# Kernel tuning notes

Hardware: AMD Instinct MI355X
Metric: run time of the kernel (lower is better)

## Reference

```python
import jax, jax.numpy as jnp
import numpy as np

N_NODES = 100000
N_EDGES = 3200000
IN_C, HID_C, OUT_C = 5, 128, 64


def setup_inputs() -> dict:
    key = jax.random.key(0)
    k_x, k_e, k_w1, k_b1, k_w2, k_b2 = jax.random.split(key, 6)
    x = jax.random.normal(k_x, (N_NODES, IN_C), dtype=jnp.float32)
    edge_index = jax.random.randint(k_e, (2, N_EDGES), 0, N_NODES, dtype=jnp.int32)
    # GCNConv learned params (glorot weights, zero-ish bias)
    W1 = jax.random.normal(k_w1, (IN_C, HID_C), dtype=jnp.float32) * (1.0 / np.sqrt(IN_C))
    b1 = jax.random.normal(k_b1, (HID_C,), dtype=jnp.float32) * 0.01
    W2 = jax.random.normal(k_w2, (HID_C, OUT_C), dtype=jnp.float32) * (1.0 / np.sqrt(HID_C))
    b2 = jax.random.normal(k_b2, (OUT_C,), dtype=jnp.float32) * 0.01
    return {"x": x, "edge_index": edge_index, "W1": W1, "b1": b1, "W2": W2, "b2": b2}


def _gcn_conv(x, src, dst, deg_inv_sqrt, W, b):
    """One GCNConv (PyG defaults: self-loops already in src/dst, symmetric norm, bias)."""
    h = x @ W                                   # [N, C_out]
    norm = deg_inv_sqrt[src] * deg_inv_sqrt[dst]  # [E+N]
    msg = h[src] * norm[:, None]                # gather + scale
    out = jax.ops.segment_sum(msg, dst, num_segments=x.shape[0])  # scatter-add
    return out + b


def reference(x, edge_index, W1, b1, W2, b2):
    n = x.shape[0]
    loop = jnp.arange(n, dtype=edge_index.dtype)
    src = jnp.concatenate([edge_index[0], loop])  # self-loops appended
    dst = jnp.concatenate([edge_index[1], loop])
    deg = jax.ops.segment_sum(jnp.ones_like(src, dtype=x.dtype), dst, num_segments=n)
    deg_inv_sqrt = jnp.where(deg > 0, jax.lax.rsqrt(deg), 0.0)
    h = _gcn_conv(x, src, dst, deg_inv_sqrt, W1, b1)
    z = _gcn_conv(h, src, dst, deg_inv_sqrt, W2, b2)
    return z
```

## Files before the change

kernel.cpp:

```cpp
#include <hip/hip_runtime.h>

#define IN_C  5
#define HID_C 128
#define OUT_C 64

#define KB   256
#define NBP  512
#define CAP  10240
#define TILE 4096
#define BTH  512
#define EPT  (TILE / BTH)
#define GNODES 64


__global__ __launch_bounds__(BTH) void k_bin(const int* __restrict__ src,
                                             const int* __restrict__ dstp,
                                             int* __restrict__ gcursor,
                                             int* __restrict__ binned, int e) {
    __shared__ int lhist[NBP];
    __shared__ int lfill[NBP];
    __shared__ int lgofs[NBP];
    __shared__ int lbeg[NBP];
    __shared__ int lsort[TILE];
    __shared__ int gdst[TILE];
    __shared__ int wsum[8];
    __shared__ int stot;
    int tid = threadIdx.x;
    int lane = tid & 63, w = tid >> 6;
    int tbeg = blockIdx.x * TILE;
    lhist[tid] = 0; lfill[tid] = 0;
    __syncthreads();
    int pk[EPT], bk[EPT];
    #pragma unroll
    for (int q = 0; q < EPT; ++q) {
        int idx = tbeg + q * BTH + tid;
        if (idx < e) {
            int s = src[idx], d = dstp[idx];
            pk[q] = ((d & 255) << 24) | s;
            bk[q] = ((unsigned)d) >> 8;
            atomicAdd(&lhist[bk[q]], 1);
        } else bk[q] = -1;
    }
    __syncthreads();
    int h = lhist[tid];
    int v = h;
    #pragma unroll
    for (int m = 1; m < 64; m <<= 1) { int u = __shfl_up(v, m); if (lane >= m) v += u; }
    if (lane == 63) wsum[w] = v;
    __syncthreads();
    if (tid == 0) {
        int s = 0;
        #pragma unroll
        for (int k = 0; k < 8; ++k) { int tv = wsum[k]; wsum[k] = s; s += tv; }
    }
    __syncthreads();
    int excl = wsum[w] + v - h;
    lbeg[tid] = excl;
    if (h > 0)
        lgofs[tid] = tid * CAP + atomicAdd(&gcursor[tid], h) - excl;
    if (tid == BTH - 1) stot = excl + h;
    __syncthreads();
    #pragma unroll
    for (int q = 0; q < EPT; ++q) {
        if (bk[q] >= 0) {
            int slot = lbeg[bk[q]] + atomicAdd(&lfill[bk[q]], 1);
            lsort[slot] = pk[q];
            gdst[slot] = lgofs[bk[q]] + slot;
        }
    }
    __syncthreads();
    int tot = stot;
    for (int i = tid; i < tot; i += BTH)
        binned[gdst[i]] = lsort[i];
}

__global__ __launch_bounds__(BTH) void k_build(int* __restrict__ binned,
                                               const int* __restrict__ gcursor,
                                               const float* __restrict__ x,
                                               int2* __restrict__ pse,
                                               float* __restrict__ xs, int n) {
    __shared__ int cnt[KB];
    __shared__ int wt[4];
    __shared__ int wte[4];
    int tid = threadIdx.x;
    int lane = tid & 63, w = tid >> 6;
    int bkt = blockIdx.x;
    int beg = bkt * CAP;
    int tot = gcursor[bkt];
    if (tid < KB) cnt[tid] = 0;
    __syncthreads();
    int4 r[5];
    #pragma unroll
    for (int it = 0; it < 5; ++it) {
        int j0 = (tid << 2) + it * (BTH * 4);
        if (j0 < tot) {
            r[it] = *(const int4*)(binned + beg + j0);
            atomicAdd(&cnt[((unsigned)r[it].x) >> 24], 1);
            if (j0 + 1 < tot) atomicAdd(&cnt[((unsigned)r[it].y) >> 24], 1);
            if (j0 + 2 < tot) atomicAdd(&cnt[((unsigned)r[it].z) >> 24], 1);
            if (j0 + 3 < tot) atomicAdd(&cnt[((unsigned)r[it].w) >> 24], 1);
        }
    }
    __syncthreads();
    int deg = (tid < KB) ? cnt[tid] : 0;
    int v = deg;
    #pragma unroll
    for (int m = 1; m < 64; m <<= 1) { int u = __shfl_up(v, m); if (lane >= m) v += u; }
    if (tid < KB && lane == 63) wt[w] = v;
    __syncthreads();
    if (tid == 0) {
        int s = 0;
        #pragma unroll
        for (int k = 0; k < 4; ++k) { wte[k] = s; s += wt[k]; }
    }
    __syncthreads();
    if (tid < KB) {
        int rel = wte[w] + v - deg;
        int node = bkt * KB + tid;
        pse[node] = make_int2(beg + rel, beg + rel + deg);
        cnt[tid] = rel;
        float d = rsqrtf(1.0f + (float)deg);
        float4 q0 = {0, 0, 0, 0}, q1 = {0, 0, 0, 0};
        if (node < n) {
            q0.x = x[node * IN_C + 0] * d;
            q0.y = x[node * IN_C + 1] * d;
            q0.z = x[node * IN_C + 2] * d;
            q0.w = x[node * IN_C + 3] * d;
            q1.x = x[node * IN_C + 4] * d;
            q1.y = d;
        }
        ((float4*)(xs + (size_t)node * 8))[0] = q0;
        ((float4*)(xs + (size_t)node * 8))[1] = q1;
    }
    __syncthreads();
    #pragma unroll
    for (int it = 0; it < 5; ++it) {
        int j0 = (tid << 2) + it * (BTH * 4);
        if (j0 < tot) {
            {
                int slot = atomicAdd(&cnt[((unsigned)r[it].x) >> 24], 1);
                binned[beg + slot] = r[it].x & 0xFFFFFF;
            }
            if (j0 + 1 < tot) {
                int slot = atomicAdd(&cnt[((unsigned)r[it].y) >> 24], 1);
                binned[beg + slot] = r[it].y & 0xFFFFFF;
            }
            if (j0 + 2 < tot) {
                int slot = atomicAdd(&cnt[((unsigned)r[it].z) >> 24], 1);
                binned[beg + slot] = r[it].z & 0xFFFFFF;
            }
            if (j0 + 3 < tot) {
                int slot = atomicAdd(&cnt[((unsigned)r[it].w) >> 24], 1);
                binned[beg + slot] = r[it].w & 0xFFFFFF;
            }
        }
    }
}

__global__ __launch_bounds__(BTH) void k_gath0(const int* __restrict__ srclist,
                                               const int2* __restrict__ pse,
                                               const float* __restrict__ feat,
                                               float* __restrict__ outf,
                                               float* __restrict__ tout, int n) {
    int tid = threadIdx.x;
    int node = blockIdx.x * GNODES + (tid >> 3);
    int sub = tid & 7;
    if (node >= n) return;
    int2 pp = pse[node];
    int ps = pp.x, pe = pp.y;
    float a0 = 0, a1 = 0, a2 = 0, a3 = 0, a4 = 0, a5 = 0;
    int j = ps + sub;
    for (; j + 24 < pe; j += 32) {
        int s0 = srclist[j],      s1 = srclist[j + 8];
        int s2 = srclist[j + 16], s3 = srclist[j + 24];
        const float* b0 = feat + (size_t)s0 * 8;
        const float* b1 = feat + (size_t)s1 * 8;
        const float* b2 = feat + (size_t)s2 * 8;
        const float* b3 = feat + (size_t)s3 * 8;
        float4 rA0 = *(const float4*)b0; float2 rA1 = *(const float2*)(b0 + 4);
        float4 rB0 = *(const float4*)b1; float2 rB1 = *(const float2*)(b1 + 4);
        float4 rC0 = *(const float4*)b2; float2 rC1 = *(const float2*)(b2 + 4);
        float4 rD0 = *(const float4*)b3; float2 rD1 = *(const float2*)(b3 + 4);
        a0 += (rA0.x + rB0.x) + (rC0.x + rD0.x);
        a1 += (rA0.y + rB0.y) + (rC0.y + rD0.y);
        a2 += (rA0.z + rB0.z) + (rC0.z + rD0.z);
        a3 += (rA0.w + rB0.w) + (rC0.w + rD0.w);
        a4 += (rA1.x + rB1.x) + (rC1.x + rD1.x);
        a5 += (rA1.y + rB1.y) + (rC1.y + rD1.y);
    }
    for (; j < pe; j += 8) {
        int sA = srclist[j];
        const float* bA = feat + (size_t)sA * 8;
        float4 rA0 = *(const float4*)bA; float2 rA1 = *(const float2*)(bA + 4);
        a0 += rA0.x; a1 += rA0.y; a2 += rA0.z; a3 += rA0.w;
        a4 += rA1.x; a5 += rA1.y;
    }
    #pragma unroll
    for (int m = 1; m < 8; m <<= 1) {
        a0 += __shfl_xor(a0, m);
        a1 += __shfl_xor(a1, m);
        a2 += __shfl_xor(a2, m);
        a3 += __shfl_xor(a3, m);
        a4 += __shfl_xor(a4, m);
        a5 += __shfl_xor(a5, m);
    }
    if (sub == 0) {
        const float4* psr = (const float4*)(feat + (size_t)node * 8);
        float4 s0 = psr[0], s1 = psr[1];
        float d = s1.y;
        a0 += s0.x; a1 += s0.y; a2 += s0.z; a3 += s0.w; a4 += s1.x;
        a5 += s1.y;
        float d2 = d * d;
        float4 o0, o1;
        o0.x = d2 * a0; o0.y = d2 * a1; o0.z = d2 * a2; o0.w = d2 * a3;
        o1.x = d2 * a4;
        o1.y = d;
        o1.z = 0.0f; o1.w = 0.0f;
        tout[node] = d * a5;
        ((float4*)(outf + (size_t)node * 8))[0] = o0;
        ((float4*)(outf + (size_t)node * 8))[1] = o1;
    }
}

__global__ __launch_bounds__(BTH) void k_gout(const int* __restrict__ srclist,
                                              const int2* __restrict__ pse,
                                              const float* __restrict__ feat,
                                              const float* __restrict__ t,
                                              const float* __restrict__ W1,
                                              const float* __restrict__ b1,
                                              const float* __restrict__ W2,
                                              const float* __restrict__ b2,
                                              float* __restrict__ out, int n) {
    __shared__ float snode[GNODES * 8];
    __shared__ float sW[IN_C * OUT_C + 2 * OUT_C];
    int tid = threadIdx.x;
    if (tid < IN_C * OUT_C) {
        int k = tid >> 6, c = tid & 63;
        float acc = 0.0f;
        for (int m = 0; m < HID_C; ++m)
            acc += W1[k * HID_C + m] * W2[m * OUT_C + c];
        sW[tid] = acc;
    } else if (tid < IN_C * OUT_C + OUT_C) {
        int c = tid - IN_C * OUT_C;
        float acc = 0.0f;
        for (int m = 0; m < HID_C; ++m)
            acc += b1[m] * W2[m * OUT_C + c];
        sW[tid] = acc;
    } else if (tid < IN_C * OUT_C + 2 * OUT_C) {
        sW[tid] = b2[tid - IN_C * OUT_C - OUT_C];
    }
    int node = blockIdx.x * GNODES + (tid >> 3);
    int sub = tid & 7;
    bool act = (node < n);
    float a0 = 0, a1 = 0, a2 = 0, a3 = 0, a4 = 0;
    if (act) {
        int2 pp = pse[node];
        int ps = pp.x, pe = pp.y;
        int j = ps + sub;
        for (; j + 24 < pe; j += 32) {
            int s0 = srclist[j],      s1 = srclist[j + 8];
            int s2 = srclist[j + 16], s3 = srclist[j + 24];
            const float* c0 = feat + (size_t)s0 * 8;
            const float* c1 = feat + (size_t)s1 * 8;
            const float* c2 = feat + (size_t)s2 * 8;
            const float* c3 = feat + (size_t)s3 * 8;
            float4 rA0 = *(const float4*)c0; float rA4 = c0[4];
            float4 rB0 = *(const float4*)c1; float rB4 = c1[4];
            float4 rC0 = *(const float4*)c2; float rC4 = c2[4];
            float4 rD0 = *(const float4*)c3; float rD4 = c3[4];
            a0 += (rA0.x + rB0.x) + (rC0.x + rD0.x);
            a1 += (rA0.y + rB0.y) + (rC0.y + rD0.y);
            a2 += (rA0.z + rB0.z) + (rC0.z + rD0.z);
            a3 += (rA0.w + rB0.w) + (rC0.w + rD0.w);
            a4 += (rA4 + rB4) + (rC4 + rD4);
        }
        for (; j < pe; j += 8) {
            int sA = srclist[j];
            const float* cA = feat + (size_t)sA * 8;
            float4 rA0 = *(const float4*)cA;
            a0 += rA0.x; a1 += rA0.y; a2 += rA0.z; a3 += rA0.w; a4 += cA[4];
        }
    }
    #pragma unroll
    for (int m = 1; m < 8; m <<= 1) {
        a0 += __shfl_xor(a0, m);
        a1 += __shfl_xor(a1, m);
        a2 += __shfl_xor(a2, m);
        a3 += __shfl_xor(a3, m);
        a4 += __shfl_xor(a4, m);
    }
    if (act && sub == 0) {
        const float4* psr = (const float4*)(feat + (size_t)node * 8);
        float4 s0 = psr[0], s1 = psr[1];
        float d = s1.y;
        a0 += s0.x; a1 += s0.y; a2 += s0.z; a3 += s0.w; a4 += s1.x;
        float* sn = snode + (tid >> 3) * 8;
        sn[0] = d * a0; sn[1] = d * a1; sn[2] = d * a2;
        sn[3] = d * a3; sn[4] = d * a4; sn[5] = t[node];
    }
    __syncthreads();
    int base = blockIdx.x * GNODES;
    for (int u = tid; u < GNODES * 16; u += BTH) {
        int ln = u >> 4, q = u & 15;
        int i = base + ln;
        if (i >= n) continue;
        const float* a = snode + ln * 8;
        float ti = a[5];
        float4 acc = ((const float4*)(sW + IN_C * OUT_C + OUT_C))[q];
        float4 bq  = ((const float4*)(sW + IN_C * OUT_C))[q];
        acc.x += ti * bq.x; acc.y += ti * bq.y;
        acc.z += ti * bq.z; acc.w += ti * bq.w;
        #pragma unroll
        for (int k = 0; k < IN_C; ++k) {
            float ak = a[k];
            float4 wk = ((const float4*)(sW + k * OUT_C))[q];
            acc.x += ak * wk.x; acc.y += ak * wk.y;
            acc.z += ak * wk.z; acc.w += ak * wk.w;
        }
        ((float4*)out)[(size_t)i * 16 + q] = acc;
    }
}

extern "C" void kernel_launch(void* const* d_in, const int* in_sizes, int n_in,
                              void* d_out, int out_size, void* d_ws, size_t ws_size,
                              hipStream_t stream) {
    const float* x   = (const float*)d_in[0];
    const int*   ei  = (const int*)d_in[1];
    const float* W1  = (const float*)d_in[2];
    const float* b1  = (const float*)d_in[3];
    const float* W2  = (const float*)d_in[4];
    const float* b2  = (const float*)d_in[5];
    float* out = (float*)d_out;

    const int n = in_sizes[0] / IN_C;
    const int e = in_sizes[1] / 2;
    const int* src = ei;
    const int* dst = ei + e;
    const int NB = (n + KB - 1) / KB;
    const int NKB = NB * KB;

    int*   gcursor = (int*)d_ws;
    int*   binned  = gcursor + 512;
    int2*  pse     = (int2*)(binned + (size_t)NBP * CAP);
    float* xs      = (float*)(pse + NKB);
    float* p1      = xs + (size_t)8 * NKB;
    float* t       = p1 + (size_t)8 * NKB;

    const int gB = (e + TILE - 1) / TILE;
    const int gG = (n + GNODES - 1) / GNODES;

    hipMemsetAsync(gcursor, 0, NBP * sizeof(int), stream);
    k_bin   <<<gB, BTH, 0, stream>>>(src, dst, gcursor, binned, e);
    k_build <<<NB, BTH, 0, stream>>>(binned, gcursor, x, pse, xs, n);
    k_gath0 <<<gG, BTH, 0, stream>>>(binned, pse, xs, p1, t, n);
    k_gout  <<<gG, BTH, 0, stream>>>(binned, pse, p1, t,
                                     W1, b1, W2, b2, out, n);
}
```

Measured before the change: 198.3 us.

## Vectorize bin loads, stage build scatter in LDS, add nontemporal loads/stores

k_bin now reads src/dst as 4-wide nontemporal vector loads instead of scalar strided loads. k_build scatters the sorted edge list into a 40KB shared staging buffer and then writes it back to global memory with coalesced stores, replacing random global scatter writes. The gather kernels load the source index list with nontemporal hints, and the output kernel uses nontemporal stores. The vector loads assume the edge count is a multiple of 4 within each tile, and the large LDS buffer may lower k_build occupancy.

```diff
diff --git a/kernel.cpp b/kernel.cpp
--- a/kernel.cpp
+++ b/kernel.cpp
@@ -10,7 +10,11 @@
 #define TILE 4096
 #define BTH  512
 #define EPT  (TILE / BTH)
+#define EPTV (TILE / BTH / 4)
 #define GNODES 64
+
+typedef int   vi4 __attribute__((ext_vector_type(4)));
+typedef float vf4 __attribute__((ext_vector_type(4)));
 
 
 __global__ __launch_bounds__(BTH) void k_bin(const int* __restrict__ src,
@@ -32,14 +36,22 @@
     __syncthreads();
     int pk[EPT], bk[EPT];
     #pragma unroll
-    for (int q = 0; q < EPT; ++q) {
-        int idx = tbeg + q * BTH + tid;
+    for (int q = 0; q < EPTV; ++q) {
+        int idx = tbeg + (q * BTH + tid) * 4;
         if (idx < e) {
-            int s = src[idx], d = dstp[idx];
-            pk[q] = ((d & 255) << 24) | s;
-            bk[q] = ((unsigned)d) >> 8;
-            atomicAdd(&lhist[bk[q]], 1);
-        } else bk[q] = -1;
+            vi4 s4 = __builtin_nontemporal_load((const vi4*)(src + idx));
+            vi4 d4 = __builtin_nontemporal_load((const vi4*)(dstp + idx));
+            pk[q*4+0] = ((d4.x & 255) << 24) | s4.x; bk[q*4+0] = ((unsigned)d4.x) >> 8;
+            pk[q*4+1] = ((d4.y & 255) << 24) | s4.y; bk[q*4+1] = ((unsigned)d4.y) >> 8;
+            pk[q*4+2] = ((d4.z & 255) << 24) | s4.z; bk[q*4+2] = ((unsigned)d4.z) >> 8;
+            pk[q*4+3] = ((d4.w & 255) << 24) | s4.w; bk[q*4+3] = ((unsigned)d4.w) >> 8;
+            atomicAdd(&lhist[bk[q*4+0]], 1);
+            atomicAdd(&lhist[bk[q*4+1]], 1);
+            atomicAdd(&lhist[bk[q*4+2]], 1);
+            atomicAdd(&lhist[bk[q*4+3]], 1);
+        } else {
+            bk[q*4+0] = -1; bk[q*4+1] = -1; bk[q*4+2] = -1; bk[q*4+3] = -1;
+        }
     }
     __syncthreads();
     int h = lhist[tid];
@@ -82,6 +94,7 @@
     __shared__ int cnt[KB];
     __shared__ int wt[4];
     __shared__ int wte[4];
+    __shared__ int stage[CAP];
     int tid = threadIdx.x;
     int lane = tid & 63, w = tid >> 6;
     int bkt = blockIdx.x;
@@ -139,22 +152,25 @@
         if (j0 < tot) {
             {
                 int slot = atomicAdd(&cnt[((unsigned)r[it].x) >> 24], 1);
-                binned[beg + slot] = r[it].x & 0xFFFFFF;
+                stage[slot] = r[it].x & 0xFFFFFF;
             }
             if (j0 + 1 < tot) {
                 int slot = atomicAdd(&cnt[((unsigned)r[it].y) >> 24], 1);
-                binned[beg + slot] = r[it].y & 0xFFFFFF;
+                stage[slot] = r[it].y & 0xFFFFFF;
             }
             if (j0 + 2 < tot) {
                 int slot = atomicAdd(&cnt[((unsigned)r[it].z) >> 24], 1);
-                binned[beg + slot] = r[it].z & 0xFFFFFF;
+                stage[slot] = r[it].z & 0xFFFFFF;
             }
             if (j0 + 3 < tot) {
                 int slot = atomicAdd(&cnt[((unsigned)r[it].w) >> 24], 1);
-                binned[beg + slot] = r[it].w & 0xFFFFFF;
+                stage[slot] = r[it].w & 0xFFFFFF;
             }
         }
     }
+    __syncthreads();
+    for (int j = tid; j < tot; j += BTH)
+        binned[beg + j] = stage[j];
 }
 
 __global__ __launch_bounds__(BTH) void k_gath0(const int* __restrict__ srclist,
@@ -171,8 +187,10 @@
     float a0 = 0, a1 = 0, a2 = 0, a3 = 0, a4 = 0, a5 = 0;
     int j = ps + sub;
     for (; j + 24 < pe; j += 32) {
-        int s0 = srclist[j],      s1 = srclist[j + 8];
-        int s2 = srclist[j + 16], s3 = srclist[j + 24];
+        int s0 = __builtin_nontemporal_load(srclist + j);
+        int s1 = __builtin_nontemporal_load(srclist + j + 8);
+        int s2 = __builtin_nontemporal_load(srclist + j + 16);
+        int s3 = __builtin_nontemporal_load(srclist + j + 24);
         const float* b0 = feat + (size_t)s0 * 8;
         const float* b1 = feat + (size_t)s1 * 8;
         const float* b2 = feat + (size_t)s2 * 8;
@@ -189,7 +207,7 @@
         a5 += (rA1.y + rB1.y) + (rC1.y + rD1.y);
     }
     for (; j < pe; j += 8) {
-        int sA = srclist[j];
+        int sA = __builtin_nontemporal_load(srclist + j);
         const float* bA = feat + (size_t)sA * 8;
         float4 rA0 = *(const float4*)bA; float2 rA1 = *(const float2*)(bA + 4);
         a0 += rA0.x; a1 += rA0.y; a2 += rA0.z; a3 += rA0.w;
@@ -258,8 +276,10 @@
         int ps = pp.x, pe = pp.y;
         int j = ps + sub;
         for (; j + 24 < pe; j += 32) {
-            int s0 = srclist[j],      s1 = srclist[j + 8];
-            int s2 = srclist[j + 16], s3 = srclist[j + 24];
+            int s0 = __builtin_nontemporal_load(srclist + j);
+            int s1 = __builtin_nontemporal_load(srclist + j + 8);
+            int s2 = __builtin_nontemporal_load(srclist + j + 16);
+            int s3 = __builtin_nontemporal_load(srclist + j + 24);
             const float* c0 = feat + (size_t)s0 * 8;
             const float* c1 = feat + (size_t)s1 * 8;
             const float* c2 = feat + (size_t)s2 * 8;
@@ -275,7 +295,7 @@
             a4 += (rA4 + rB4) + (rC4 + rD4);
         }
         for (; j < pe; j += 8) {
-            int sA = srclist[j];
+            int sA = __builtin_nontemporal_load(srclist + j);
             const float* cA = feat + (size_t)sA * 8;
             float4 rA0 = *(const float4*)cA;
             a0 += rA0.x; a1 += rA0.y; a2 += rA0.z; a3 += rA0.w; a4 += cA[4];
@@ -317,7 +337,8 @@
             acc.x += ak * wk.x; acc.y += ak * wk.y;
             acc.z += ak * wk.z; acc.w += ak * wk.w;
         }
-        ((float4*)out)[(size_t)i * 16 + q] = acc;
+        vf4 av; av.x = acc.x; av.y = acc.y; av.z = acc.z; av.w = acc.w;
+        __builtin_nontemporal_store(av, ((vf4*)out) + (size_t)i * 16 + q);
     }
 }
 
@@ -349,7 +370,7 @@
     const int gB = (e + TILE - 1) / TILE;
     const int gG = (n + GNODES - 1) / GNODES;
 
-    hipMemsetAsync(gcursor, 0, NBP * sizeof(int), stream);
+    (void)hipMemsetAsync(gcursor, 0, NBP * sizeof(int), stream);
     k_bin   <<<gB, BTH, 0, stream>>>(src, dst, gcursor, binned, e);
     k_build <<<NB, BTH, 0, stream>>>(binned, gcursor, x, pse, xs, n);
     k_gath0 <<<gG, BTH, 0, stream>>>(binned, pse, xs, p1, t, n);
```

Measured after the change: 205.9 us. 3.9% more time.
